# Kernel tuning notes

Hardware: AMD Instinct MI355X
Metric: run time of the kernel (lower is better)

Reference implementation:

```python
import jax, jax.numpy as jnp
import numpy as np

HID = 4096
HEADS = 32
HEAD_DIM = 128
SEQ = 2048
GROUP = 128          # AWQ quantization group size along the input (K) dim
QKV_OUT = 3 * HID
ROPE_BASE = 10000.0


def dequant(qweight, scales, zeros):
    # qweight: [K, N] int; scales/zeros: [K//GROUP, N]
    s = jnp.repeat(scales, GROUP, axis=0)
    z = jnp.repeat(zeros, GROUP, axis=0)
    return (qweight.astype(jnp.float32) - z) * s


def rotate_half(x):
    x1, x2 = jnp.split(x, 2, axis=-1)
    return jnp.concatenate((-x2, x1), axis=-1)


def setup_inputs() -> dict:
    key = jax.random.key(0)
    ks = jax.random.split(key, 8)
    hidden_states = jax.random.normal(ks[0], (1, SEQ, HID), dtype=jnp.float32)
    position_ids = jnp.arange(SEQ, dtype=jnp.int32)[None, :]
    qkv_qweight = jax.random.randint(ks[1], (HID, QKV_OUT), 0, 16, dtype=jnp.int32)
    qkv_scales = jax.random.uniform(ks[2], (HID // GROUP, QKV_OUT), dtype=jnp.float32) * 0.002
    qkv_zeros = jax.random.uniform(ks[3], (HID // GROUP, QKV_OUT), dtype=jnp.float32) * 16.0
    o_qweight = jax.random.randint(ks[4], (HID, HID), 0, 16, dtype=jnp.int32)
    o_scales = jax.random.uniform(ks[5], (HID // GROUP, HID), dtype=jnp.float32) * 0.002
    o_zeros = jax.random.uniform(ks[6], (HID // GROUP, HID), dtype=jnp.float32) * 16.0
    return {"hidden_states": hidden_states, "position_ids": position_ids,
            "qkv_qweight": qkv_qweight, "qkv_scales": qkv_scales, "qkv_zeros": qkv_zeros,
            "o_qweight": o_qweight, "o_scales": o_scales, "o_zeros": o_zeros}


def reference(hidden_states, position_ids, qkv_qweight, qkv_scales, qkv_zeros,
              o_qweight, o_scales, o_zeros):
    b, s, _ = hidden_states.shape
    # --- quantized QKV projection (dequant + GEMM) ---
    w_qkv = dequant(qkv_qweight, qkv_scales, qkv_zeros)        # [HID, 3*HID]
    proj = jnp.einsum('bsk,kn->bsn', hidden_states, w_qkv)     # [b, s, 3*HID]
    xqkv = proj.reshape(b, s, 3, HEADS, HEAD_DIM)
    # [b, h, s, d]
    q = jnp.transpose(xqkv[:, :, 0], (0, 2, 1, 3))
    k = jnp.transpose(xqkv[:, :, 1], (0, 2, 1, 3))
    v = jnp.transpose(xqkv[:, :, 2], (0, 2, 1, 3))
    # --- rotary embedding (no KV cache: kv_seq_len == s) ---
    inv_freq = 1.0 / (ROPE_BASE ** (jnp.arange(0, HEAD_DIM, 2, dtype=jnp.float32) / HEAD_DIM))
    t = jnp.arange(s, dtype=jnp.float32)
    freqs = jnp.outer(t, inv_freq)                             # [s, d/2]
    emb = jnp.concatenate((freqs, freqs), axis=-1)             # [s, d]
    cos = jnp.cos(emb)[position_ids][:, None]                  # [b, 1, s, d]
    sin = jnp.sin(emb)[position_ids][:, None]
    q = q * cos + rotate_half(q) * sin
    k = k * cos + rotate_half(k) * sin
    # --- causal attention (flash_attn_func, padding_mask=None branch) ---
    scale = 1.0 / jnp.sqrt(jnp.float32(HEAD_DIM))
    scores = jnp.einsum('bhqd,bhkd->bhqk', q, k) * scale       # [b, h, s, s]
    causal = jnp.tril(jnp.ones((s, s), dtype=bool))
    scores = jnp.where(causal, scores, jnp.float32(-1e30))
    probs = jax.nn.softmax(scores, axis=-1)
    attn = jnp.einsum('bhqk,bhkd->bhqd', probs, v)             # [b, h, s, d]
    attn = jnp.transpose(attn, (0, 2, 1, 3)).reshape(b, s, HID)
    # --- quantized output projection ---
    w_o = dequant(o_qweight, o_scales, o_zeros)                # [HID, HID]
    out = jnp.einsum('bsk,kn->bsn', attn, w_o)                 # [b, s, HID]
    return out
```

## Files before the change

kernel.cpp:

```cpp
#include <hip/hip_runtime.h>
#include <hip/hip_bf16.h>

#define S_LEN 2048
#define HID_DIM 4096
#define NH 32
#define HD 128
#define NQKV 12288

typedef _Float16 half2v __attribute__((ext_vector_type(2)));
typedef _Float16 half4v __attribute__((ext_vector_type(4)));
typedef _Float16 half8v __attribute__((ext_vector_type(8)));
typedef float f32x4 __attribute__((ext_vector_type(4)));

typedef const __attribute__((address_space(1))) unsigned int* gas_u32;
typedef __attribute__((address_space(3))) unsigned int* las_u32;

__device__ inline void g2lds16(const _Float16* g, _Float16* l) {
  __builtin_amdgcn_global_load_lds((gas_u32)g, (las_u32)l, 16, 0, 0);
}

__global__ __launch_bounds__(256) void dequant_w(const int* __restrict__ W,
                                                 const float* __restrict__ scal,
                                                 const float* __restrict__ zer,
                                                 _Float16* __restrict__ Wt, int K, int N) {
  __shared__ _Float16 lT[64 * 84];
  const int k0 = blockIdx.y * 64, n0 = blockIdx.x * 64;
  const int tid = threadIdx.x, c = tid & 63, rp = tid >> 6;
  const int g = k0 >> 7;
  const float sc = scal[(size_t)g * N + n0 + c];
  const float zp = zer[(size_t)g * N + n0 + c];
#pragma unroll
  for (int i = 0; i < 8; ++i) {
    const int k = i * 8 + rp * 2;
    const float q0 = (float)W[(size_t)(k0 + k) * N + n0 + c];
    const float q1 = (float)W[(size_t)(k0 + k + 1) * N + n0 + c];
    half2v p;
    p[0] = (_Float16)((q0 - zp) * sc);
    p[1] = (_Float16)((q1 - zp) * sc);
    *(half2v*)&lT[c * 84 + k] = p;
  }
  __syncthreads();
  const int kc = tid & 7, nr0 = tid >> 3;
#pragma unroll
  for (int i = 0; i < 2; ++i) {
    const int n = nr0 + 32 * i;
    union { half8v v8; half4v v4[2]; } u;
    u.v4[0] = *(const half4v*)&lT[n * 84 + kc * 8];
    u.v4[1] = *(const half4v*)&lT[n * 84 + kc * 8 + 4];
    *(half8v*)&Wt[(size_t)(n0 + n) * K + k0 + kc * 8] = u.v8;
  }
}

__global__ __launch_bounds__(256) void conv_a(const float* __restrict__ A, _Float16* __restrict__ Af) {
  const int i = blockIdx.x * 256 + threadIdx.x;
  const float4 t = ((const float4*)A)[i];
  half4v r;
  r[0] = (_Float16)t.x; r[1] = (_Float16)t.y; r[2] = (_Float16)t.z; r[3] = (_Float16)t.w;
  ((half4v*)Af)[i] = r;
}

__device__ inline void stage128x64(const _Float16* __restrict__ gp, int K,
                                   _Float16* lp, int wave, int stR, int stC) {
  g2lds16(gp + (size_t)(wave * 16 + stR) * K + stC, lp + (wave * 2) * 512);
  g2lds16(gp + (size_t)(wave * 16 + 8 + stR) * K + stC, lp + (wave * 2 + 1) * 512);
}

template <typename CT>
__global__ __launch_bounds__(512, 2) void gemm_f16(const _Float16* __restrict__ A,
                                                   const _Float16* __restrict__ Bt,
                                                   CT* __restrict__ C, int M, int N, int K) {
  __shared__ _Float16 sA[3][2][128 * 64];
  __shared__ _Float16 sB[2][128 * 64];

  const int tid = threadIdx.x;
  const int wave = tid >> 6, lane = tid & 63;
  const int quad = lane >> 4, l16 = lane & 15;
  const int wr = wave >> 2;
  const int wc = wave & 3;
  const int NT = K >> 6;

  const _Float16* Ab = A + (size_t)(blockIdx.y * 256) * K;
  const _Float16* Bb = Bt + (size_t)(blockIdx.x * 128) * K;

  const int stR = lane >> 3;
  const int stC = ((lane & 7) ^ stR) << 3;
  const int fx = l16 & 7;

#define LDA8(buf, half, r, c) (*(const half8v*)&sA[buf][half][(r) * 64 + (((c) ^ fx) << 3)])
#define LDB8(buf, r, c) (*(const half8v*)&sB[buf][(r) * 64 + (((c) ^ fx) << 3)])

  f32x4 acc[8][2];
  const f32x4 zero4 = {0.f, 0.f, 0.f, 0.f};
#pragma unroll
  for (int am = 0; am < 8; ++am)
#pragma unroll
    for (int nb = 0; nb < 2; ++nb) acc[am][nb] = zero4;

  stage128x64(Ab, K, &sA[0][0][0], wave, stR, stC);
  stage128x64(Ab + (size_t)128 * K, K, &sA[0][1][0], wave, stR, stC);
  stage128x64(Bb, K, &sB[0][0], wave, stR, stC);
  stage128x64(Ab + 64, K, &sA[1][0][0], wave, stR, stC);
  stage128x64(Ab + (size_t)128 * K + 64, K, &sA[1][1][0], wave, stR, stC);
  stage128x64(Bb + 64, K, &sB[1][0], wave, stR, stC);
  asm volatile("s_waitcnt vmcnt(6)" ::: "memory");
  __builtin_amdgcn_s_barrier();

  int bA = 0;
  for (int t = 0; t < NT; ++t) {
    const int bB = t & 1;
    const int bA2 = (bA + 2 >= 3) ? bA - 1 : bA + 2;

    half8v af[4][2], bf[2][2];
#pragma unroll
    for (int mb = 0; mb < 4; ++mb)
#pragma unroll
      for (int ks = 0; ks < 2; ++ks)
        af[mb][ks] = LDA8(bA, wr, mb * 16 + l16, ks * 4 + quad);
#pragma unroll
    for (int nb = 0; nb < 2; ++nb)
#pragma unroll
      for (int ks = 0; ks < 2; ++ks)
        bf[nb][ks] = LDB8(bB, wc * 32 + nb * 16 + l16, ks * 4 + quad);
    if (t + 2 < NT) {
      const _Float16* Ap = Ab + (size_t)(t + 2) * 64;
      stage128x64(Ap, K, &sA[bA2][0][0], wave, stR, stC);
      stage128x64(Ap + (size_t)128 * K, K, &sA[bA2][1][0], wave, stR, stC);
    }
    __builtin_amdgcn_s_barrier();
    asm volatile("s_waitcnt lgkmcnt(0)" ::: "memory");
    __builtin_amdgcn_sched_barrier(0);
    __builtin_amdgcn_s_setprio(1);
#pragma unroll
    for (int mb = 0; mb < 4; ++mb)
#pragma unroll
      for (int nb = 0; nb < 2; ++nb)
#pragma unroll
        for (int ks = 0; ks < 2; ++ks)
          acc[mb][nb] =
              __builtin_amdgcn_mfma_f32_16x16x32_f16(af[mb][ks], bf[nb][ks], acc[mb][nb], 0, 0, 0);
    __builtin_amdgcn_s_setprio(0);
    __builtin_amdgcn_s_barrier();

#pragma unroll
    for (int mb = 0; mb < 4; ++mb)
#pragma unroll
      for (int ks = 0; ks < 2; ++ks)
        af[mb][ks] = LDA8(bA, wr, 64 + mb * 16 + l16, ks * 4 + quad);
    if (t + 2 < NT) {
      stage128x64(Bb + (size_t)(t + 2) * 64, K, &sB[bB][0], wave, stR, stC);
      asm volatile("s_waitcnt vmcnt(6)" ::: "memory");
    } else if (t + 1 < NT) {
      asm volatile("s_waitcnt vmcnt(0)" ::: "memory");
    }
    __builtin_amdgcn_s_barrier();
    asm volatile("s_waitcnt lgkmcnt(0)" ::: "memory");
    __builtin_amdgcn_sched_barrier(0);
    __builtin_amdgcn_s_setprio(1);
#pragma unroll
    for (int mb = 0; mb < 4; ++mb)
#pragma unroll
      for (int nb = 0; nb < 2; ++nb)
#pragma unroll
        for (int ks = 0; ks < 2; ++ks)
          acc[4 + mb][nb] = __builtin_amdgcn_mfma_f32_16x16x32_f16(af[mb][ks], bf[nb][ks],
                                                                   acc[4 + mb][nb], 0, 0, 0);
    __builtin_amdgcn_s_setprio(0);
    __builtin_amdgcn_s_barrier();

    bA = (bA + 1 >= 3) ? 0 : bA + 1;
  }

  const int rbase = blockIdx.y * 256 + wr * 128 + quad * 4;
  const int cbase = blockIdx.x * 128 + wc * 32 + l16;
#pragma unroll
  for (int am = 0; am < 8; ++am)
#pragma unroll
    for (int nb = 0; nb < 2; ++nb)
#pragma unroll
      for (int i = 0; i < 4; ++i)
        C[(size_t)(rbase + am * 16 + i) * N + cbase + nb * 16] = (CT)acc[am][nb][i];
#undef LDA8
#undef LDB8
}

__global__ __launch_bounds__(256) void rope_kernel(const _Float16* __restrict__ proj,
                                                   const int* __restrict__ pos,
                                                   _Float16* __restrict__ Q, _Float16* __restrict__ K,
                                                   _Float16* __restrict__ Vt) {
  const int h = blockIdx.x, sb = blockIdx.y;
  const int tid = threadIdx.x;
  const int s0 = sb * 64;

#pragma unroll
  for (int it = 0; it < 16; ++it) {
    const int idx = it * 256 + tid;
    const int sl = idx >> 6, j = idx & 63;
    const int s = s0 + sl;
    const float p = (float)pos[s];
    const float invrev = exp2f(-0.20762050593045455f * (float)j) * 0.15915494309189535f;
    const float rev = p * invrev;
    const float frac = rev - floorf(rev);
    const float sn = __builtin_amdgcn_sinf(frac);
    const float cs = __builtin_amdgcn_cosf(frac);
    const _Float16* rp = proj + (size_t)s * NQKV + h * HD;
    {
      const float x1 = (float)rp[j], x2 = (float)rp[j + 64];
      _Float16* qp = Q + ((size_t)h * S_LEN + s) * HD;
      qp[j] = (_Float16)(x1 * cs - x2 * sn);
      qp[j + 64] = (_Float16)(x2 * cs + x1 * sn);
    }
    {
      const float x1 = (float)rp[HID_DIM + j], x2 = (float)rp[HID_DIM + j + 64];
      _Float16* kp = K + ((size_t)h * S_LEN + s) * HD;
      kp[j] = (_Float16)(x1 * cs - x2 * sn);
      kp[j + 64] = (_Float16)(x2 * cs + x1 * sn);
    }
  }

  __shared__ _Float16 lV[64 * 132];
#pragma unroll
  for (int r = 0; r < 4; ++r) {
    const int cid = r * 256 + tid;
    const int sl = cid >> 4;
    const int d0 = (cid & 15) * 8;
    const _Float16* vp = proj + (size_t)(s0 + sl) * NQKV + 2 * HID_DIM + h * HD + d0;
    *(half4v*)&lV[sl * 132 + d0] = *(const half4v*)vp;
    *(half4v*)&lV[sl * 132 + d0 + 4] = *(const half4v*)(vp + 4);
  }
  __syncthreads();
#pragma unroll
  for (int it = 0; it < 32; ++it) {
    const int d = it * 4 + (tid >> 6);
    const int sl = tid & 63;
    Vt[((size_t)h * HD + d) * S_LEN + s0 + sl] = lV[sl * 132 + d];
  }
}

__global__ __launch_bounds__(256) void flash_attn(const _Float16* __restrict__ Q,
                                                  const _Float16* __restrict__ Km,
                                                  const _Float16* __restrict__ Vt,
                                                  _Float16* __restrict__ O) {
  __shared__ _Float16 lK[32 * 128];
  __shared__ _Float16 lV[128 * 32];
  __shared__ _Float16 lP[4][2][16 * 40];
  const int h = blockIdx.y;
  const int xb = blockIdx.x;
  const int qb = (xb & 1) ? (15 - (xb >> 1)) : (xb >> 1);
  const int tid = threadIdx.x;
  const int wave = tid >> 6, lane = tid & 63;
  const int quad = lane >> 4, l16 = lane & 15;
  const int q0w = qb * 128 + wave * 32;
  const float scale = 0.08838834764831845f;

  const _Float16* Qh = Q + (size_t)h * S_LEN * HD;
  const _Float16* Kh = Km + (size_t)h * S_LEN * HD;
  const _Float16* Vh = Vt + (size_t)h * HD * S_LEN;

  const int kRow0 = wave * 8 + (lane >> 4);
  const int kSlot = lane & 15;
  const int vRow0 = wave * 32 + (lane >> 2);
  const int vSlot = lane & 3;

  half8v qf[2][4];
#pragma unroll
  for (int r = 0; r < 2; ++r)
#pragma unroll
    for (int c = 0; c < 4; ++c)
      qf[r][c] = *(const half8v*)&Qh[(size_t)(q0w + r * 16 + l16) * HD + c * 32 + quad * 8];

  const f32x4 zero4 = {0.f, 0.f, 0.f, 0.f};
  f32x4 o[2][8];
  f32x4 lp[2];
#pragma unroll
  for (int r = 0; r < 2; ++r) {
    lp[r] = zero4;
#pragma unroll
    for (int c = 0; c < 8; ++c) o[r][c] = zero4;
  }

  const int ntiles = 4 * qb + 4;
  for (int kt = 0; kt < ntiles; ++kt) {
#pragma unroll
    for (int i = 0; i < 2; ++i) {
      const int row = kRow0 + i * 4;
      const int ck = kSlot ^ (row & 15);
      g2lds16(Kh + (size_t)(kt * 32 + row) * HD + ck * 8, &lK[(wave * 8 + i * 4) * 128]);
    }
#pragma unroll
    for (int i = 0; i < 2; ++i) {
      const int row = vRow0 + i * 16;
      const int cv = vSlot ^ ((row >> 1) & 3);
      g2lds16(Vh + (size_t)row * S_LEN + kt * 32 + cv * 8, &lV[(wave * 32 + i * 16) * 32]);
    }
    __syncthreads();

    half8v kf[2][4];
#pragma unroll
    for (int hf = 0; hf < 2; ++hf)
#pragma unroll
      for (int c = 0; c < 4; ++c) {
        const int slot = (c * 4 + quad) ^ l16;
        kf[hf][c] = *(const half8v*)&lK[(hf * 16 + l16) * 128 + slot * 8];
      }
    half8v vf[8];
#pragma unroll
    for (int c = 0; c < 8; ++c) {
      const int slot = quad ^ ((l16 >> 1) & 3);
      vf[c] = *(const half8v*)&lV[(c * 16 + l16) * 32 + slot * 8];
    }

    f32x4 s[2][2];
#pragma unroll
    for (int r = 0; r < 2; ++r)
#pragma unroll
      for (int hf = 0; hf < 2; ++hf) {
        s[r][hf] = zero4;
#pragma unroll
        for (int c = 0; c < 4; ++c)
          s[r][hf] = __builtin_amdgcn_mfma_f32_16x16x32_f16(qf[r][c], kf[hf][c], s[r][hf], 0, 0, 0);
      }

#pragma unroll
    for (int r = 0; r < 2; ++r) {
      float p0[4], p1[4];
#pragma unroll
      for (int i = 0; i < 4; ++i) {
        const int row = q0w + r * 16 + quad * 4 + i;
        const int col0 = kt * 32 + l16, col1 = col0 + 16;
        const float e0 = __expf(s[r][0][i] * scale);
        const float e1 = __expf(s[r][1][i] * scale);
        p0[i] = (col0 <= row) ? e0 : 0.f;
        p1[i] = (col1 <= row) ? e1 : 0.f;
        lp[r][i] += p0[i] + p1[i];
      }
      _Float16* pw = lP[wave][r];
#pragma unroll
      for (int i = 0; i < 4; ++i) {
        pw[(quad * 4 + i) * 40 + l16] = (_Float16)p0[i];
        pw[(quad * 4 + i) * 40 + l16 + 16] = (_Float16)p1[i];
      }
    }
    half8v pa[2];
#pragma unroll
    for (int r = 0; r < 2; ++r) pa[r] = *(half8v*)&lP[wave][r][l16 * 40 + quad * 8];

#pragma unroll
    for (int c = 0; c < 8; ++c)
#pragma unroll
      for (int r = 0; r < 2; ++r)
        o[r][c] = __builtin_amdgcn_mfma_f32_16x16x32_f16(pa[r], vf[c], o[r][c], 0, 0, 0);

    __syncthreads();
  }

#pragma unroll
  for (int r = 0; r < 2; ++r) {
    f32x4 ls = lp[r];
#pragma unroll
    for (int off = 1; off < 16; off <<= 1) {
#pragma unroll
      for (int i = 0; i < 4; ++i) ls[i] += __shfl_xor(ls[i], off);
    }
    f32x4 inv;
#pragma unroll
    for (int i = 0; i < 4; ++i) inv[i] = 1.f / ls[i];
#pragma unroll
    for (int c = 0; c < 8; ++c) {
#pragma unroll
      for (int i = 0; i < 4; ++i) {
        const int row = q0w + r * 16 + quad * 4 + i;
        O[(size_t)row * HID_DIM + h * HD + c * 16 + l16] = (_Float16)(o[r][c][i] * inv[i]);
      }
    }
  }
}

extern "C" void kernel_launch(void* const* d_in, const int* in_sizes, int n_in,
                              void* d_out, int out_size, void* d_ws, size_t ws_size,
                              hipStream_t stream) {
  const float* hidden = (const float*)d_in[0];
  const int* pos = (const int*)d_in[1];
  const int* qkv_w = (const int*)d_in[2];
  const float* qkv_s = (const float*)d_in[3];
  const float* qkv_z = (const float*)d_in[4];
  const int* o_w = (const int*)d_in[5];
  const float* o_s = (const float*)d_in[6];
  const float* o_z = (const float*)d_in[7];

  char* ws = (char*)d_ws;
  _Float16* Wt_qkv = (_Float16*)(ws + 0);
  _Float16* Qb = (_Float16*)(ws + 0);
  _Float16* Kb = (_Float16*)(ws + 16777216);
  _Float16* Vtb = (_Float16*)(ws + 33554432);
  _Float16* Af16 = (_Float16*)(ws + 100663296);
  _Float16* attn = (_Float16*)(ws + 100663296);
  _Float16* proj = (_Float16*)(ws + 117440512);
  _Float16* Wt_o = (_Float16*)(ws + 117440512);
  float* out = (float*)d_out;

  hipLaunchKernelGGL(dequant_w, dim3(192, 64), dim3(256), 0, stream,
                     qkv_w, qkv_s, qkv_z, Wt_qkv, 4096, 12288);
  hipLaunchKernelGGL(conv_a, dim3(8192), dim3(256), 0, stream, hidden, Af16);
  hipLaunchKernelGGL((gemm_f16<_Float16>), dim3(96, 8), dim3(512), 0, stream,
                     Af16, Wt_qkv, proj, 2048, 12288, 4096);
  hipLaunchKernelGGL(rope_kernel, dim3(32, 32), dim3(256), 0, stream, proj, pos, Qb, Kb, Vtb);
  hipLaunchKernelGGL(dequant_w, dim3(64, 64), dim3(256), 0, stream,
                     o_w, o_s, o_z, Wt_o, 4096, 4096);
  hipLaunchKernelGGL(flash_attn, dim3(16, 32), dim3(256), 0, stream, Qb, Kb, Vtb, attn);
  hipLaunchKernelGGL((gemm_f16<float>), dim3(32, 8), dim3(512), 0, stream,
                     attn, Wt_o, out, 2048, 4096, 4096);
}
```

Before: 770.1 us.

## Add dedicated 256x384-tile QKV GEMM with interleaved double-buffered staging

```diff
diff --git a/kernel.cpp b/kernel.cpp
--- a/kernel.cpp
+++ b/kernel.cpp
@@ -57,6 +57,128 @@
   half4v r;
   r[0] = (_Float16)t.x; r[1] = (_Float16)t.y; r[2] = (_Float16)t.z; r[3] = (_Float16)t.w;
   ((half4v*)Af)[i] = r;
+}
+
+__global__ __launch_bounds__(512, 2) void gemm_qkv(const _Float16* __restrict__ A,
+                                                   const _Float16* __restrict__ Bt,
+                                                   _Float16* __restrict__ C, int M, int N, int K) {
+  __shared__ _Float16 sA[2][256 * 64];
+  __shared__ _Float16 sB[2][384 * 64];
+
+  const int tid = threadIdx.x;
+  const int wave = tid >> 6, lane = tid & 63;
+  const int quad = lane >> 4, l16 = lane & 15;
+  const int wr = wave >> 2;
+  const int wc = wave & 3;
+  const int NT = K >> 6;
+
+  const _Float16* Ab = A + (size_t)(blockIdx.y * 256) * K;
+  const _Float16* Bb = Bt + (size_t)(blockIdx.x * 384) * K;
+
+  const int sRow = tid >> 3;
+  const size_t sOff = (size_t)sRow * K + (((tid & 7) ^ (sRow & 7)) << 3);
+  const _Float16* Asrc = Ab + sOff;
+  const _Float16* Bsrc = Bb + sOff;
+  const int ldst = wave * 512;
+
+  const int fx = l16 & 7;
+  const int aBase = (wr * 128 + l16) * 64;
+  const int bBase = (wc * 96 + l16) * 64;
+  const int cOff0 = ((quad ^ fx) << 3);
+  const int cOff1 = (((4 + quad) ^ fx) << 3);
+
+  f32x4 acc[8][6];
+  const f32x4 zero4 = {0.f, 0.f, 0.f, 0.f};
+#pragma unroll
+  for (int m8 = 0; m8 < 8; ++m8)
+#pragma unroll
+    for (int nb = 0; nb < 6; ++nb) acc[m8][nb] = zero4;
+
+#define STAGE_A(t_, j_) g2lds16(Asrc + (size_t)(j_) * 64 * K + (size_t)(t_) * 64, \
+                                &sA[(t_) & 1][(j_) * 4096 + ldst])
+#define STAGE_B(t_, j_) g2lds16(Bsrc + (size_t)(j_) * 64 * K + (size_t)(t_) * 64, \
+                                &sB[(t_) & 1][(j_) * 4096 + ldst])
+
+  STAGE_A(0, 0); STAGE_A(0, 2);
+  STAGE_B(0, 0); STAGE_B(0, 1); STAGE_B(0, 2);
+  STAGE_B(0, 3); STAGE_B(0, 4); STAGE_B(0, 5);
+  STAGE_A(0, 1); STAGE_A(0, 3);
+  asm volatile("s_waitcnt vmcnt(2)" ::: "memory");
+  __builtin_amdgcn_s_barrier();
+
+  for (int t = 0; t < NT; ++t) {
+    const int rs = (t & 1);
+    const int slotA = rs * 16384, slotB = rs * 24576;
+    const bool pf = (t + 1 < NT);
+    half8v af[4], bf[6];
+
+#define READ_A(mbh_, co_)                                                              \
+  _Pragma("unroll") for (int mb = 0; mb < 4; ++mb)                                     \
+      af[mb] = *(const half8v*)&sA[0][slotA + aBase + (mbh_)*4096 + mb * 1024 + (co_)];
+#define READ_B(co_)                                                                    \
+  _Pragma("unroll") for (int nb = 0; nb < 6; ++nb)                                     \
+      bf[nb] = *(const half8v*)&sB[0][slotB + bBase + nb * 1024 + (co_)];
+#define MFMA24(mbh_)                                                                   \
+  __builtin_amdgcn_s_setprio(1);                                                       \
+  _Pragma("unroll") for (int mb = 0; mb < 4; ++mb)                                     \
+      _Pragma("unroll") for (int nb = 0; nb < 6; ++nb)                                 \
+          acc[(mbh_)*4 + mb][nb] =                                                     \
+              __builtin_amdgcn_mfma_f32_16x16x32_f16(af[mb], bf[nb], acc[(mbh_)*4 + mb][nb], 0, 0, 0); \
+  __builtin_amdgcn_s_setprio(0);
+
+    READ_A(0, cOff0)
+    READ_B(cOff0)
+    if (pf) { STAGE_A(t + 1, 0); STAGE_A(t + 1, 2); }
+    if (pf) { asm volatile("s_waitcnt vmcnt(2)" ::: "memory"); }
+    else    { asm volatile("s_waitcnt vmcnt(0)" ::: "memory"); }
+    __builtin_amdgcn_s_barrier();
+    asm volatile("s_waitcnt lgkmcnt(0)" ::: "memory");
+    __builtin_amdgcn_sched_barrier(0);
+    MFMA24(0)
+
+    READ_A(1, cOff0)
+    if (pf) { STAGE_B(t + 1, 0); STAGE_B(t + 1, 1); STAGE_B(t + 1, 2); }
+    __builtin_amdgcn_s_barrier();
+    asm volatile("s_waitcnt lgkmcnt(0)" ::: "memory");
+    __builtin_amdgcn_sched_barrier(0);
+    MFMA24(1)
+
+    READ_A(0, cOff1)
+    READ_B(cOff1)
+    if (pf) { STAGE_B(t + 1, 3); STAGE_B(t + 1, 4); STAGE_B(t + 1, 5); }
+    __builtin_amdgcn_s_barrier();
+    asm volatile("s_waitcnt lgkmcnt(0)" ::: "memory");
+    __builtin_amdgcn_sched_barrier(0);
+    MFMA24(0)
+
+    READ_A(1, cOff1)
+    if (pf) {
+      STAGE_A(t + 1, 1); STAGE_A(t + 1, 3);
+      asm volatile("s_waitcnt vmcnt(2)" ::: "memory");
+    }
+    __builtin_amdgcn_s_barrier();
+    asm volatile("s_waitcnt lgkmcnt(0)" ::: "memory");
+    __builtin_amdgcn_sched_barrier(0);
+    MFMA24(1)
+
+#undef READ_A
+#undef READ_B
+#undef MFMA24
+  }
+
+  const int rbase = blockIdx.y * 256 + wr * 128 + quad * 4;
+  const int cbase = blockIdx.x * 384 + wc * 96 + l16;
+#pragma unroll
+  for (int m8 = 0; m8 < 8; ++m8) {
+    const int rowb = rbase + (m8 >> 2) * 64 + (m8 & 3) * 16;
+#pragma unroll
+    for (int nb = 0; nb < 6; ++nb)
+#pragma unroll
+      for (int i = 0; i < 4; ++i)
+        C[(size_t)(rowb + i) * N + cbase + nb * 16] = (_Float16)acc[m8][nb][i];
+  }
+#undef STAGE_A
+#undef STAGE_B
 }
 
 __device__ inline void stage128x64(const _Float16* __restrict__ gp, int K,
@@ -401,7 +523,7 @@
   hipLaunchKernelGGL(dequant_w, dim3(192, 64), dim3(256), 0, stream,
                      qkv_w, qkv_s, qkv_z, Wt_qkv, 4096, 12288);
   hipLaunchKernelGGL(conv_a, dim3(8192), dim3(256), 0, stream, hidden, Af16);
-  hipLaunchKernelGGL((gemm_f16<_Float16>), dim3(96, 8), dim3(512), 0, stream,
+  hipLaunchKernelGGL(gemm_qkv, dim3(32, 8), dim3(512), 0, stream,
                      Af16, Wt_qkv, proj, 2048, 12288, 4096);
   hipLaunchKernelGGL(rope_kernel, dim3(32, 32), dim3(256), 0, stream, proj, pos, Qb, Kb, Vtb);
   hipLaunchKernelGGL(dequant_w, dim3(64, 64), dim3(256), 0, stream,
```

Result: slower. 818.4 us (+6.3%).

## Add 256x256-tile QKV GEMM kernel with double-buffered B staging

Applied to the files above, without the earlier changes.

```diff
diff --git a/kernel.cpp b/kernel.cpp
--- a/kernel.cpp
+++ b/kernel.cpp
@@ -63,6 +63,130 @@
                                    _Float16* lp, int wave, int stR, int stC) {
   g2lds16(gp + (size_t)(wave * 16 + stR) * K + stC, lp + (wave * 2) * 512);
   g2lds16(gp + (size_t)(wave * 16 + 8 + stR) * K + stC, lp + (wave * 2 + 1) * 512);
+}
+
+__global__ __launch_bounds__(512, 2) void gemm_qkv(const _Float16* __restrict__ A,
+                                                   const _Float16* __restrict__ Bt,
+                                                   _Float16* __restrict__ C, int M, int N, int K) {
+  __shared__ _Float16 sA[3][2][128 * 64];
+  __shared__ _Float16 sB[2][2][128 * 64];
+
+  const int tid = threadIdx.x;
+  const int wave = tid >> 6, lane = tid & 63;
+  const int quad = lane >> 4, l16 = lane & 15;
+  const int wr = wave >> 2;
+  const int wc = wave & 3;
+  const int NT = K >> 6;
+
+  const _Float16* Ab = A + (size_t)(blockIdx.y * 256) * K;
+  const _Float16* Bb = Bt + (size_t)(blockIdx.x * 256) * K;
+
+  const int stR = lane >> 3;
+  const int stC = ((lane & 7) ^ stR) << 3;
+  const int fx = l16 & 7;
+  const int bHalf = wc >> 1;
+  const int bRow0 = (wc & 1) * 64;
+
+#define COFF(ks_) ((((ks_)*4 + quad) ^ fx) << 3)
+#define LDA8(r_, ks_) (*(const half8v*)&sA[bA][wr][(r_) * 64 + COFF(ks_)])
+#define LDB8(r_, ks_) (*(const half8v*)&sB[bB][bHalf][(r_) * 64 + COFF(ks_)])
+
+  f32x4 acc[8][4];
+  const f32x4 zero4 = {0.f, 0.f, 0.f, 0.f};
+#pragma unroll
+  for (int m8 = 0; m8 < 8; ++m8)
+#pragma unroll
+    for (int nb = 0; nb < 4; ++nb) acc[m8][nb] = zero4;
+
+  stage128x64(Ab, K, &sA[0][0][0], wave, stR, stC);
+  stage128x64(Ab + (size_t)128 * K, K, &sA[0][1][0], wave, stR, stC);
+  stage128x64(Bb, K, &sB[0][0][0], wave, stR, stC);
+  stage128x64(Bb + (size_t)128 * K, K, &sB[0][1][0], wave, stR, stC);
+  stage128x64(Ab + 64, K, &sA[1][0][0], wave, stR, stC);
+  stage128x64(Ab + (size_t)128 * K + 64, K, &sA[1][1][0], wave, stR, stC);
+  stage128x64(Bb + 64, K, &sB[1][0][0], wave, stR, stC);
+  stage128x64(Bb + (size_t)128 * K + 64, K, &sB[1][1][0], wave, stR, stC);
+  asm volatile("s_waitcnt vmcnt(8)" ::: "memory");
+  __builtin_amdgcn_s_barrier();
+
+  int bA = 0;
+  for (int t = 0; t < NT; ++t) {
+    const int bB = t & 1;
+    const int bA2 = (bA + 2 >= 3) ? bA - 1 : bA + 2;
+
+    half8v af[4][2], bf[4][2];
+#pragma unroll
+    for (int mb = 0; mb < 4; ++mb)
+#pragma unroll
+      for (int ks = 0; ks < 2; ++ks) af[mb][ks] = LDA8(mb * 16 + l16, ks);
+#pragma unroll
+    for (int nb = 0; nb < 4; ++nb)
+#pragma unroll
+      for (int ks = 0; ks < 2; ++ks) bf[nb][ks] = LDB8(bRow0 + nb * 16 + l16, ks);
+    if (t + 2 < NT) {
+      const _Float16* Ap = Ab + (size_t)(t + 2) * 64;
+      stage128x64(Ap, K, &sA[bA2][0][0], wave, stR, stC);
+      stage128x64(Ap + (size_t)128 * K, K, &sA[bA2][1][0], wave, stR, stC);
+    }
+    __builtin_amdgcn_s_barrier();
+    asm volatile("s_waitcnt lgkmcnt(0)" ::: "memory");
+    __builtin_amdgcn_sched_barrier(0);
+    __builtin_amdgcn_s_setprio(1);
+#pragma unroll
+    for (int mb = 0; mb < 4; ++mb)
+#pragma unroll
+      for (int nb = 0; nb < 4; ++nb)
+#pragma unroll
+        for (int ks = 0; ks < 2; ++ks)
+          acc[mb][nb] =
+              __builtin_amdgcn_mfma_f32_16x16x32_f16(af[mb][ks], bf[nb][ks], acc[mb][nb], 0, 0, 0);
+    __builtin_amdgcn_s_setprio(0);
+    __builtin_amdgcn_s_barrier();
+
+#pragma unroll
+    for (int mb = 0; mb < 4; ++mb)
+#pragma unroll
+      for (int ks = 0; ks < 2; ++ks) af[mb][ks] = LDA8(64 + mb * 16 + l16, ks);
+    if (t + 2 < NT) {
+      const _Float16* Bp = Bb + (size_t)(t + 2) * 64;
+      stage128x64(Bp, K, &sB[bB][0][0], wave, stR, stC);
+      stage128x64(Bp + (size_t)128 * K, K, &sB[bB][1][0], wave, stR, stC);
+      asm volatile("s_waitcnt vmcnt(8)" ::: "memory");
+    } else if (t + 1 < NT) {
+      asm volatile("s_waitcnt vmcnt(0)" ::: "memory");
+    }
+    __builtin_amdgcn_s_barrier();
+    asm volatile("s_waitcnt lgkmcnt(0)" ::: "memory");
+    __builtin_amdgcn_sched_barrier(0);
+    __builtin_amdgcn_s_setprio(1);
+#pragma unroll
+    for (int mb = 0; mb < 4; ++mb)
+#pragma unroll
+      for (int nb = 0; nb < 4; ++nb)
+#pragma unroll
+        for (int ks = 0; ks < 2; ++ks)
+          acc[4 + mb][nb] = __builtin_amdgcn_mfma_f32_16x16x32_f16(af[mb][ks], bf[nb][ks],
+                                                                   acc[4 + mb][nb], 0, 0, 0);
+    __builtin_amdgcn_s_setprio(0);
+    __builtin_amdgcn_s_barrier();
+
+    bA = (bA + 1 >= 3) ? 0 : bA + 1;
+  }
+
+  const int rbase = blockIdx.y * 256 + wr * 128 + quad * 4;
+  const int cbase = blockIdx.x * 256 + wc * 64 + l16;
+#pragma unroll
+  for (int m8 = 0; m8 < 8; ++m8) {
+    const int rowb = rbase + (m8 >> 2) * 64 + (m8 & 3) * 16;
+#pragma unroll
+    for (int nb = 0; nb < 4; ++nb)
+#pragma unroll
+      for (int i = 0; i < 4; ++i)
+        C[(size_t)(rowb + i) * N + cbase + nb * 16] = (_Float16)acc[m8][nb][i];
+  }
+#undef COFF
+#undef LDA8
+#undef LDB8
 }
 
 template <typename CT>
@@ -401,7 +525,7 @@
   hipLaunchKernelGGL(dequant_w, dim3(192, 64), dim3(256), 0, stream,
                      qkv_w, qkv_s, qkv_z, Wt_qkv, 4096, 12288);
   hipLaunchKernelGGL(conv_a, dim3(8192), dim3(256), 0, stream, hidden, Af16);
-  hipLaunchKernelGGL((gemm_f16<_Float16>), dim3(96, 8), dim3(512), 0, stream,
+  hipLaunchKernelGGL(gemm_qkv, dim3(48, 8), dim3(512), 0, stream,
                      Af16, Wt_qkv, proj, 2048, 12288, 4096);
   hipLaunchKernelGGL(rope_kernel, dim3(32, 32), dim3(256), 0, stream, proj, pos, Qb, Kb, Vtb);
   hipLaunchKernelGGL(dequant_w, dim3(64, 64), dim3(256), 0, stream,
```

Result: no change. 773.5 us (+0.4%).

## Restructure GEMM into four-phase pipeline with 256x256 tiles for QKV

Applied to the files above, without the earlier changes.

```diff
diff --git a/kernel.cpp b/kernel.cpp
--- a/kernel.cpp
+++ b/kernel.cpp
@@ -65,12 +65,13 @@
   g2lds16(gp + (size_t)(wave * 16 + 8 + stR) * K + stC, lp + (wave * 2 + 1) * 512);
 }
 
-template <typename CT>
-__global__ __launch_bounds__(512, 2) void gemm_f16(const _Float16* __restrict__ A,
+template <int NB, typename CT>
+__global__ __launch_bounds__(512, 2) void gemm_4ph(const _Float16* __restrict__ A,
                                                    const _Float16* __restrict__ Bt,
                                                    CT* __restrict__ C, int M, int N, int K) {
+  constexpr int NBH = NB / 2;
   __shared__ _Float16 sA[3][2][128 * 64];
-  __shared__ _Float16 sB[2][128 * 64];
+  __shared__ _Float16 sB[2][NBH][128 * 64];
 
   const int tid = threadIdx.x;
   const int wave = tid >> 6, lane = tid & 63;
@@ -80,107 +81,120 @@
   const int NT = K >> 6;
 
   const _Float16* Ab = A + (size_t)(blockIdx.y * 256) * K;
-  const _Float16* Bb = Bt + (size_t)(blockIdx.x * 128) * K;
+  const _Float16* Bb = Bt + (size_t)(blockIdx.x * (NB * 64)) * K;
 
   const int stR = lane >> 3;
   const int stC = ((lane & 7) ^ stR) << 3;
   const int fx = l16 & 7;
-
-#define LDA8(buf, half, r, c) (*(const half8v*)&sA[buf][half][(r) * 64 + (((c) ^ fx) << 3)])
-#define LDB8(buf, r, c) (*(const half8v*)&sB[buf][(r) * 64 + (((c) ^ fx) << 3)])
-
-  f32x4 acc[8][2];
+  const int bh = (NB == 4) ? (wc >> 1) : 0;
+  const int brow0 = (NB == 4) ? ((wc & 1) * 64) : (wc * 32);
+
+#define COFF(ks_) ((((ks_) * 4 + quad) ^ fx) << 3)
+#define SYNC_MFMA()                                  \
+  __builtin_amdgcn_s_barrier();                      \
+  asm volatile("s_waitcnt lgkmcnt(0)" ::: "memory"); \
+  __builtin_amdgcn_sched_barrier(0);
+#define MFMA_Q(moff_, noff_, bfr_)                                                       \
+  __builtin_amdgcn_s_setprio(1);                                                         \
+  _Pragma("unroll") for (int mb = 0; mb < 4; ++mb)                                       \
+  _Pragma("unroll") for (int nb = 0; nb < NBH; ++nb)                                     \
+  _Pragma("unroll") for (int ks = 0; ks < 2; ++ks)                                       \
+      acc[(moff_) + mb][(noff_) + nb] = __builtin_amdgcn_mfma_f32_16x16x32_f16(          \
+          af[mb][ks], bfr_[nb][ks], acc[(moff_) + mb][(noff_) + nb], 0, 0, 0);           \
+  __builtin_amdgcn_s_setprio(0);
+
+  f32x4 acc[8][NB];
   const f32x4 zero4 = {0.f, 0.f, 0.f, 0.f};
 #pragma unroll
-  for (int am = 0; am < 8; ++am)
-#pragma unroll
-    for (int nb = 0; nb < 2; ++nb) acc[am][nb] = zero4;
-
+  for (int m8 = 0; m8 < 8; ++m8)
+#pragma unroll
+    for (int nb = 0; nb < NB; ++nb) acc[m8][nb] = zero4;
+
+  stage128x64(Bb, K, &sB[0][0][0], wave, stR, stC);
+  if constexpr (NB == 4)
+    stage128x64(Bb + (size_t)128 * K, K, &sB[0][1][0], wave, stR, stC);
   stage128x64(Ab, K, &sA[0][0][0], wave, stR, stC);
   stage128x64(Ab + (size_t)128 * K, K, &sA[0][1][0], wave, stR, stC);
-  stage128x64(Bb, K, &sB[0][0], wave, stR, stC);
   stage128x64(Ab + 64, K, &sA[1][0][0], wave, stR, stC);
   stage128x64(Ab + (size_t)128 * K + 64, K, &sA[1][1][0], wave, stR, stC);
-  stage128x64(Bb + 64, K, &sB[1][0], wave, stR, stC);
-  asm volatile("s_waitcnt vmcnt(6)" ::: "memory");
+  asm volatile("s_waitcnt vmcnt(4)" ::: "memory");
   __builtin_amdgcn_s_barrier();
 
   int bA = 0;
   for (int t = 0; t < NT; ++t) {
     const int bB = t & 1;
     const int bA2 = (bA + 2 >= 3) ? bA - 1 : bA + 2;
-
-    half8v af[4][2], bf[2][2];
+    half8v af[4][2], blo[NBH][2], bhi[NBH][2];
+
 #pragma unroll
     for (int mb = 0; mb < 4; ++mb)
 #pragma unroll
       for (int ks = 0; ks < 2; ++ks)
-        af[mb][ks] = LDA8(bA, wr, mb * 16 + l16, ks * 4 + quad);
-#pragma unroll
-    for (int nb = 0; nb < 2; ++nb)
+        af[mb][ks] = *(const half8v*)&sA[bA][wr][(mb * 16 + l16) * 64 + COFF(ks)];
+#pragma unroll
+    for (int nb = 0; nb < NBH; ++nb)
 #pragma unroll
       for (int ks = 0; ks < 2; ++ks)
-        bf[nb][ks] = LDB8(bB, wc * 32 + nb * 16 + l16, ks * 4 + quad);
+        blo[nb][ks] = *(const half8v*)&sB[bB][bh][(brow0 + nb * 16 + l16) * 64 + COFF(ks)];
+    if (t + 1 < NT)
+      stage128x64(Bb + (size_t)(t + 1) * 64, K, &sB[bB ^ 1][0][0], wave, stR, stC);
+    SYNC_MFMA()
+    MFMA_Q(0, 0, blo)
+    __builtin_amdgcn_s_barrier();
+
+#pragma unroll
+    for (int nb = 0; nb < NBH; ++nb)
+#pragma unroll
+      for (int ks = 0; ks < 2; ++ks)
+        bhi[nb][ks] =
+            *(const half8v*)&sB[bB][bh][(brow0 + (NBH + nb) * 16 + l16) * 64 + COFF(ks)];
+    if constexpr (NB == 4) {
+      if (t + 1 < NT)
+        stage128x64(Bb + (size_t)128 * K + (size_t)(t + 1) * 64, K, &sB[bB ^ 1][1][0], wave,
+                    stR, stC);
+    }
+    SYNC_MFMA()
+    MFMA_Q(0, NBH, bhi)
+    __builtin_amdgcn_s_barrier();
+
+#pragma unroll
+    for (int mb = 0; mb < 4; ++mb)
+#pragma unroll
+      for (int ks = 0; ks < 2; ++ks)
+        af[mb][ks] = *(const half8v*)&sA[bA][wr][((64 + mb * 16 + l16)) * 64 + COFF(ks)];
+    if (t + 2 < NT)
+      stage128x64(Ab + (size_t)(t + 2) * 64, K, &sA[bA2][0][0], wave, stR, stC);
+    SYNC_MFMA()
+    MFMA_Q(4, NBH, bhi)
+    __builtin_amdgcn_s_barrier();
+
     if (t + 2 < NT) {
-      const _Float16* Ap = Ab + (size_t)(t + 2) * 64;
-      stage128x64(Ap, K, &sA[bA2][0][0], wave, stR, stC);
-      stage128x64(Ap + (size_t)128 * K, K, &sA[bA2][1][0], wave, stR, stC);
-    }
+      stage128x64(Ab + (size_t)128 * K + (size_t)(t + 2) * 64, K, &sA[bA2][1][0], wave, stR, stC);
+      asm volatile("s_waitcnt vmcnt(4)" ::: "memory");
+    } else {
+      asm volatile("s_waitcnt vmcnt(0)" ::: "memory");
+    }
+    SYNC_MFMA()
+    MFMA_Q(4, 0, blo)
     __builtin_amdgcn_s_barrier();
-    asm volatile("s_waitcnt lgkmcnt(0)" ::: "memory");
-    __builtin_amdgcn_sched_barrier(0);
-    __builtin_amdgcn_s_setprio(1);
-#pragma unroll
-    for (int mb = 0; mb < 4; ++mb)
-#pragma unroll
-      for (int nb = 0; nb < 2; ++nb)
-#pragma unroll
-        for (int ks = 0; ks < 2; ++ks)
-          acc[mb][nb] =
-              __builtin_amdgcn_mfma_f32_16x16x32_f16(af[mb][ks], bf[nb][ks], acc[mb][nb], 0, 0, 0);
-    __builtin_amdgcn_s_setprio(0);
-    __builtin_amdgcn_s_barrier();
-
-#pragma unroll
-    for (int mb = 0; mb < 4; ++mb)
-#pragma unroll
-      for (int ks = 0; ks < 2; ++ks)
-        af[mb][ks] = LDA8(bA, wr, 64 + mb * 16 + l16, ks * 4 + quad);
-    if (t + 2 < NT) {
-      stage128x64(Bb + (size_t)(t + 2) * 64, K, &sB[bB][0], wave, stR, stC);
-      asm volatile("s_waitcnt vmcnt(6)" ::: "memory");
-    } else if (t + 1 < NT) {
-      asm volatile("s_waitcnt vmcnt(0)" ::: "memory");
-    }
-    __builtin_amdgcn_s_barrier();
-    asm volatile("s_waitcnt lgkmcnt(0)" ::: "memory");
-    __builtin_amdgcn_sched_barrier(0);
-    __builtin_amdgcn_s_setprio(1);
-#pragma unroll
-    for (int mb = 0; mb < 4; ++mb)
-#pragma unroll
-      for (int nb = 0; nb < 2; ++nb)
-#pragma unroll
-        for (int ks = 0; ks < 2; ++ks)
-          acc[4 + mb][nb] = __builtin_amdgcn_mfma_f32_16x16x32_f16(af[mb][ks], bf[nb][ks],
-                                                                   acc[4 + mb][nb], 0, 0, 0);
-    __builtin_amdgcn_s_setprio(0);
-    __builtin_amdgcn_s_barrier();
 
     bA = (bA + 1 >= 3) ? 0 : bA + 1;
   }
 
   const int rbase = blockIdx.y * 256 + wr * 128 + quad * 4;
-  const int cbase = blockIdx.x * 128 + wc * 32 + l16;
-#pragma unroll
-  for (int am = 0; am < 8; ++am)
-#pragma unroll
-    for (int nb = 0; nb < 2; ++nb)
+  const int cbase = blockIdx.x * (NB * 64) + wc * (NB * 16) + l16;
+#pragma unroll
+  for (int m8 = 0; m8 < 8; ++m8) {
+    const int rowb = rbase + (m8 >> 2) * 64 + (m8 & 3) * 16;
+#pragma unroll
+    for (int nb = 0; nb < NB; ++nb)
 #pragma unroll
       for (int i = 0; i < 4; ++i)
-        C[(size_t)(rbase + am * 16 + i) * N + cbase + nb * 16] = (CT)acc[am][nb][i];
-#undef LDA8
-#undef LDB8
+        C[(size_t)(rowb + i) * N + cbase + nb * 16] = (CT)acc[m8][nb][i];
+  }
+#undef COFF
+#undef SYNC_MFMA
+#undef MFMA_Q
 }
 
 __global__ __launch_bounds__(256) void rope_kernel(const _Float16* __restrict__ proj,
@@ -401,12 +415,12 @@
   hipLaunchKernelGGL(dequant_w, dim3(192, 64), dim3(256), 0, stream,
                      qkv_w, qkv_s, qkv_z, Wt_qkv, 4096, 12288);
   hipLaunchKernelGGL(conv_a, dim3(8192), dim3(256), 0, stream, hidden, Af16);
-  hipLaunchKernelGGL((gemm_f16<_Float16>), dim3(96, 8), dim3(512), 0, stream,
+  hipLaunchKernelGGL((gemm_4ph<4, _Float16>), dim3(48, 8), dim3(512), 0, stream,
                      Af16, Wt_qkv, proj, 2048, 12288, 4096);
   hipLaunchKernelGGL(rope_kernel, dim3(32, 32), dim3(256), 0, stream, proj, pos, Qb, Kb, Vtb);
   hipLaunchKernelGGL(dequant_w, dim3(64, 64), dim3(256), 0, stream,
                      o_w, o_s, o_z, Wt_o, 4096, 4096);
   hipLaunchKernelGGL(flash_attn, dim3(16, 32), dim3(256), 0, stream, Qb, Kb, Vtb, attn);
-  hipLaunchKernelGGL((gemm_f16<float>), dim3(32, 8), dim3(512), 0, stream,
+  hipLaunchKernelGGL((gemm_4ph<2, float>), dim3(32, 8), dim3(512), 0, stream,
                      attn, Wt_o, out, 2048, 4096, 4096);
 }
```

Result: slower. 807.5 us (+4.9%).
